# Kernel optimization log

Hardware: AMD Instinct MI355X
Metric: run time of the kernel (lower is better)

Reference implementation:

```python
import jax, jax.numpy as jnp
import numpy as np

B, N = 8, 16384
NPOINT, RADIUS, NSAMPLE, IN_CH = 512, 0.5, 64, 6
EPS = 1e-5


def _sqdist(a, b):
    # a [B,S,3], b [B,N,3] -> [B,S,N] squared euclidean distances
    return (jnp.sum(a * a, -1)[:, :, None] + jnp.sum(b * b, -1)[:, None, :]
            - 2.0 * jnp.einsum('bsd,bnd->bsn', a, b))


def _fps(xyz, npoint):
    # farthest point sampling (deterministic: starts from index 0)
    Bb, Nn, _ = xyz.shape
    def body(carry, _):
        dist, far = carry  # dist [B,N], far [B]
        centroid = jnp.take_along_axis(xyz, far[:, None, None], axis=1)  # [B,1,3]
        d = jnp.sum((xyz - centroid) ** 2, -1)
        dist = jnp.minimum(dist, d)
        return (dist, jnp.argmax(dist, -1).astype(jnp.int32)), far
    init = (jnp.full((Bb, Nn), 1e10, xyz.dtype), jnp.zeros((Bb,), jnp.int32))
    _, idx = jax.lax.scan(body, init, None, length=npoint)
    return idx.T  # [B, npoint]


def _ball_query(radius, nsample, xyz, new_xyz):
    Nn = xyz.shape[1]
    sq = _sqdist(new_xyz, xyz)  # [B,S,N]
    gidx = jnp.where(sq > radius * radius, Nn,
                     jnp.arange(Nn, dtype=jnp.int32)[None, None, :])
    gidx = jnp.sort(gidx, axis=-1)[:, :, :nsample]  # [B,S,K]
    # pad slots (==N) get the first valid index, as in reference torch code
    return jnp.where(gidx == Nn, gidx[:, :, :1], gidx)


def _gather(x, idx):
    # x [B,N,C], idx [B,...] -> [B,...,C]
    return jax.vmap(lambda xb, ib: xb[ib])(x, idx)


def _forward(xyz, points, layers):
    fps_idx = _fps(xyz, NPOINT)
    new_xyz = _gather(xyz, fps_idx)                        # [B,S,3]
    idx = _ball_query(RADIUS, NSAMPLE, xyz, new_xyz)       # [B,S,K]
    grouped_xyz = _gather(xyz, idx) - new_xyz[:, :, None]  # [B,S,K,3]
    grouped_pts = _gather(points, idx)                     # [B,S,K,3]
    h = jnp.concatenate([grouped_xyz, grouped_pts], -1)[..., :IN_CH]  # [B,S,K,6]
    for (W, b, g, beta) in layers:
        # 1x1 Conv2d == per-point linear; BatchNorm2d (train mode) over (B,K,S)
        h = jnp.einsum('bskc,oc->bsko', h, W) + b
        mu = jnp.mean(h, axis=(0, 1, 2))
        var = jnp.var(h, axis=(0, 1, 2))
        h = jax.nn.relu(g * (h - mu) * jax.lax.rsqrt(var + EPS) + beta)
    return new_xyz, jnp.max(h, axis=2)  # [B,S,3], [B,S,C_out]


def setup_inputs() -> dict:
    key = jax.random.key(0)
    ks = jax.random.split(key, 4)
    return {
        'xyz': jax.random.normal(ks[0], (B, N, 3), jnp.float32),
        'points': jax.random.normal(ks[1], (B, N, 3), jnp.float32),
        'W0': jax.random.normal(ks[2], (64, IN_CH), jnp.float32) * (1.0 / np.sqrt(IN_CH)),
        'b0': jnp.zeros((64,), jnp.float32),
        'g0': jnp.ones((64,), jnp.float32),
        'beta0': jnp.zeros((64,), jnp.float32),
        'W1': jax.random.normal(ks[3], (128, 64), jnp.float32) * (1.0 / np.sqrt(64)),
        'b1': jnp.zeros((128,), jnp.float32),
        'g1': jnp.ones((128,), jnp.float32),
        'beta1': jnp.zeros((128,), jnp.float32),
    }


def reference(xyz, points, W0, b0, g0, beta0, W1, b1, g1, beta1):
    layers = [(W0, b0, g0, beta0), (W1, b1, g1, beta1)]
    return _forward(xyz, points, layers)
```

## Files before the change

kernel.cpp:

```cpp
#include <hip/hip_runtime.h>

#define NB    8
#define NPTS  16384
#define NS    512
#define NK    64
#define C1    64
#define C2    128
#define RAD2  0.25f
#define MTOT  (NB*NS*NK)

typedef float v2f __attribute__((ext_vector_type(2)));
typedef __bf16 bfv8 __attribute__((ext_vector_type(8)));
typedef float f32x4 __attribute__((ext_vector_type(4)));

extern __shared__ char dynsmem[];

#define UMAX_DPP(x, CTRL, RM)                                                   \
    do {                                                                        \
        unsigned _m = (unsigned)__builtin_amdgcn_update_dpp((int)(x), (int)(x), \
                                                            CTRL, RM, 0xf, false); \
        x = (x > _m) ? x : _m;                                                  \
    } while (0)
#define UMIN_DPP(x, CTRL, RM)                                                   \
    do {                                                                        \
        unsigned _m = (unsigned)__builtin_amdgcn_update_dpp((int)(x), (int)(x), \
                                                            CTRL, RM, 0xf, false); \
        x = (x < _m) ? x : _m;                                                  \
    } while (0)

__global__ __launch_bounds__(1024, 4) void fps_kernel(const float* __restrict__ xyz,
                                                      float* __restrict__ out) {
#pragma clang fp contract(off)
    int b = blockIdx.x;
    int tid = threadIdx.x;
    int lane = tid & 63;
    int w = tid >> 6;
    const float* base = xyz + (size_t)b * NPTS * 3;
    v2f* yv = (v2f*)dynsmem;
    v2f* zv = yv + 8192;
    __shared__ unsigned svals[2][16];
    __shared__ float4 sred4[2][16];
    v2f pxp[8], ddp[8];
#pragma unroll
    for (int jj = 0; jj < 8; ++jj) {
        int p0 = tid + (jj << 11);
        int p1 = p0 + 1024;
        float x0 = base[p0 * 3 + 0], y0 = base[p0 * 3 + 1], z0 = base[p0 * 3 + 2];
        float x1 = base[p1 * 3 + 0], y1 = base[p1 * 3 + 1], z1 = base[p1 * 3 + 2];
        pxp[jj].x = x0; pxp[jj].y = x1;
        v2f yp; yp.x = y0; yp.y = y1;
        v2f zp; zp.x = z0; zp.y = z1;
        yv[(jj << 10) + tid] = yp;
        zv[(jj << 10) + tid] = zp;
        ddp[jj].x = 1e10f; ddp[jj].y = 1e10f;
    }
    float cx = base[0], cy = base[1], cz = base[2];
    if (tid == 0) {
        float* o = out + (size_t)b * NS * 3;
        o[0] = cx; o[1] = cy; o[2] = cz;
    }
    __syncthreads();
    for (int i = 1; i < NS; ++i) {
        v2f cx2; cx2.x = cx; cx2.y = cx;
        v2f cy2; cy2.x = cy; cy2.y = cy;
        v2f cz2; cz2.x = cz; cz2.y = cz;
        v2f cm0, cm1, cm2, cm3;
        cm0.x = -1.f; cm0.y = -1.f; cm1 = cm0; cm2 = cm0; cm3 = cm0;
#pragma unroll
        for (int jj = 0; jj < 8; ++jj) {
            v2f yp = yv[(jj << 10) + tid];
            v2f zp = zv[(jj << 10) + tid];
            v2f dx = pxp[jj] - cx2;
            v2f dy = yp - cy2;
            v2f dz = zp - cz2;
            v2f d = (dx * dx + dy * dy) + dz * dz;
            v2f nd;
            nd.x = fminf(ddp[jj].x, d.x);
            nd.y = fminf(ddp[jj].y, d.y);
            ddp[jj] = nd;
            if ((jj & 3) == 0) { cm0.x = fmaxf(cm0.x, nd.x); cm0.y = fmaxf(cm0.y, nd.y); }
            if ((jj & 3) == 1) { cm1.x = fmaxf(cm1.x, nd.x); cm1.y = fmaxf(cm1.y, nd.y); }
            if ((jj & 3) == 2) { cm2.x = fmaxf(cm2.x, nd.x); cm2.y = fmaxf(cm2.y, nd.y); }
            if ((jj & 3) == 3) { cm3.x = fmaxf(cm3.x, nd.x); cm3.y = fmaxf(cm3.y, nd.y); }
        }
        v2f m01; m01.x = fmaxf(cm0.x, cm1.x); m01.y = fmaxf(cm0.y, cm1.y);
        v2f m23; m23.x = fmaxf(cm2.x, cm3.x); m23.y = fmaxf(cm2.y, cm3.y);
        float bv = fmaxf(fmaxf(m01.x, m23.x), fmaxf(m01.y, m23.y));
        unsigned vb = (unsigned)__float_as_int(bv);
        UMAX_DPP(vb, 0xB1, 0xf);
        UMAX_DPP(vb, 0x4E, 0xf);
        UMAX_DPP(vb, 0x141, 0xf);
        UMAX_DPP(vb, 0x140, 0xf);
        UMAX_DPP(vb, 0x142, 0xa);
        UMAX_DPP(vb, 0x143, 0xc);
        if (lane == 63) svals[i & 1][w] = vb;
        __syncthreads();
        unsigned wv = svals[i & 1][lane & 15];
        UMAX_DPP(wv, 0xB1, 0xf);
        UMAX_DPP(wv, 0x4E, 0xf);
        UMAX_DPP(wv, 0x141, 0xf);
        UMAX_DPP(wv, 0x140, 0xf);
        float W = __int_as_float((int)wv);
        if (__any(bv == W)) {
            unsigned lidx = 0x7fffffffu;
            float lx = 0.f;
#pragma unroll
            for (int jj = 7; jj >= 0; --jj) {
                if (ddp[jj].y == W) { lidx = (unsigned)(tid + (jj << 11) + 1024); lx = pxp[jj].y; }
                if (ddp[jj].x == W) { lidx = (unsigned)(tid + (jj << 11));        lx = pxp[jj].x; }
            }
            unsigned lm = (lidx == 0x7fffffffu) ? 0u : lidx;
            unsigned slot = ((lm >> 11) << 10) + (lm & 1023u);
            unsigned e4 = ((lm >> 10) & 1u) << 2;
            float ly = *(const float*)((const char*)yv + (size_t)slot * 8 + e4);
            float lz = *(const float*)((const char*)zv + (size_t)slot * 8 + e4);
            unsigned widx = lidx;
            UMIN_DPP(widx, 0xB1, 0xf);
            UMIN_DPP(widx, 0x4E, 0xf);
            UMIN_DPP(widx, 0x141, 0xf);
            UMIN_DPP(widx, 0x140, 0xf);
            UMIN_DPP(widx, 0x142, 0xa);
            UMIN_DPP(widx, 0x143, 0xc);
            unsigned wu = (unsigned)__builtin_amdgcn_readlane((int)widx, 63);
            unsigned long long mk = __ballot(lidx == wu);
            int sl = (int)(__ffsll(mk) - 1);
            float sx = __int_as_float(__builtin_amdgcn_readlane(__float_as_int(lx), sl));
            float sy = __int_as_float(__builtin_amdgcn_readlane(__float_as_int(ly), sl));
            float sz = __int_as_float(__builtin_amdgcn_readlane(__float_as_int(lz), sl));
            if (lane == 0) sred4[i & 1][w] = make_float4(__int_as_float((int)wu), sx, sy, sz);
        } else {
            if (lane == 0) sred4[i & 1][w] = make_float4(__int_as_float(0x7fffffff), 0.f, 0.f, 0.f);
        }
        __syncthreads();
        float4 s4 = sred4[i & 1][lane & 15];
        unsigned ci = (unsigned)__float_as_int(s4.x);
        UMIN_DPP(ci, 0xB1, 0xf);
        UMIN_DPP(ci, 0x4E, 0xf);
        UMIN_DPP(ci, 0x141, 0xf);
        UMIN_DPP(ci, 0x140, 0xf);
        unsigned long long mk2 = __ballot((unsigned)__float_as_int(s4.x) == ci);
        int sl2 = (int)(__ffsll(mk2) - 1);
        cx = __int_as_float(__builtin_amdgcn_readlane(__float_as_int(s4.y), sl2));
        cy = __int_as_float(__builtin_amdgcn_readlane(__float_as_int(s4.z), sl2));
        cz = __int_as_float(__builtin_amdgcn_readlane(__float_as_int(s4.w), sl2));
        if (tid == 0) {
            float* o = out + ((size_t)b * NS + i) * 3;
            o[0] = cx; o[1] = cy; o[2] = cz;
        }
    }
}

__global__ __launch_bounds__(256) void ballq_kernel(const float* __restrict__ xyz,
                                                    const float* __restrict__ pts,
                                                    const float* __restrict__ newxyz,
                                                    float* __restrict__ feat) {
    int w = threadIdx.x >> 6;
    int lane = threadIdx.x & 63;
    int wid = blockIdx.x * 4 + w;
    int b = wid >> 9;
    const float* nx = newxyz + (size_t)wid * 3;
    float cx = nx[0], cy = nx[1], cz = nx[2];
    float sa = __fadd_rn(__fadd_rn(__fmul_rn(cx, cx), __fmul_rn(cy, cy)),
                         __fmul_rn(cz, cz));
    __shared__ int sidx[4][64];
    const float* base = xyz + (size_t)b * NPTS * 3;
    int cnt = 0;
    for (int off = 0; off < NPTS && cnt < NK; off += 64) {
        int p = off + lane;
        float bx = base[p * 3 + 0], by = base[p * 3 + 1], bz = base[p * 3 + 2];
        float sb = __fadd_rn(__fadd_rn(__fmul_rn(bx, bx), __fmul_rn(by, by)),
                             __fmul_rn(bz, bz));
        float dt = __fadd_rn(__fadd_rn(__fmul_rn(cx, bx), __fmul_rn(cy, by)),
                             __fmul_rn(cz, bz));
        float sq = __fsub_rn(__fadd_rn(sa, sb), __fmul_rn(2.0f, dt));
        bool inb = !(sq > RAD2);
        unsigned long long mask = __ballot(inb);
        int pos = cnt + (int)__popcll(mask & ((1ull << lane) - 1ull));
        if (inb && pos < NK) sidx[w][pos] = p;
        cnt += (int)__popcll(mask);
    }
    __syncthreads();
    int filled = cnt < NK ? cnt : NK;
    int sel = (lane < filled) ? lane : 0;
    int p = (filled > 0) ? sidx[w][sel] : 0;
    float gx = base[p * 3 + 0], gy = base[p * 3 + 1], gz = base[p * 3 + 2];
    const float* pb = pts + (size_t)b * NPTS * 3;
    float q0 = pb[p * 3 + 0], q1 = pb[p * 3 + 1], q2 = pb[p * 3 + 2];
    float* fr = feat + ((size_t)wid * NK + lane) * 6;
    fr[0] = __fsub_rn(gx, cx);
    fr[1] = __fsub_rn(gy, cy);
    fr[2] = __fsub_rn(gz, cz);
    fr[3] = q0; fr[4] = q1; fr[5] = q2;
}

__global__ __launch_bounds__(256) void stats0_kernel(const float* __restrict__ feat,
                                                     const float* __restrict__ W0,
                                                     const float* __restrict__ b0,
                                                     float* __restrict__ stats) {
    int lane = threadIdx.x & 63;
    int wid = blockIdx.x * 4 + (threadIdx.x >> 6);
    float w0[6];
#pragma unroll
    for (int j = 0; j < 6; ++j) w0[j] = W0[lane * 6 + j];
    float bb = b0[lane];
    float ssum = 0.f, ssq = 0.f;
    int r0 = wid * 256;
    for (int r = r0; r < r0 + 256; ++r) {
        const float* f = feat + (size_t)r * 6;
        float h = bb;
#pragma unroll
        for (int j = 0; j < 6; ++j) h = fmaf(w0[j], f[j], h);
        ssum += h;
        ssq = fmaf(h, h, ssq);
    }
    atomicAdd(&stats[lane], ssum);
    atomicAdd(&stats[64 + lane], ssq);
}

__global__ void fin0_kernel(const float* __restrict__ g0, const float* __restrict__ be0,
                            float* __restrict__ stats) {
    int c = threadIdx.x;
    const float inv = 1.0f / (float)MTOT;
    float mu = stats[c] * inv;
    float var = fmaxf(stats[64 + c] * inv - mu * mu, 0.f);
    float a = g0[c] * rsqrtf(var + 1e-5f);
    stats[384 + c] = a;
    stats[448 + c] = fmaf(-mu, a, be0[c]);
}

__global__ __launch_bounds__(256) void stats1_kernel(const float* __restrict__ feat,
                                                     const float* __restrict__ W0,
                                                     const float* __restrict__ b0,
                                                     const float* __restrict__ W1,
                                                     const float* __restrict__ b1,
                                                     float* __restrict__ stats) {
    int lane = threadIdx.x & 63;
    int w = threadIdx.x >> 6;
    int half = w & 1;
    int pairG = blockIdx.x * 2 + (w >> 1);
    int ch = half * 64 + lane;
    float w0r[6];
#pragma unroll
    for (int j = 0; j < 6; ++j) w0r[j] = W0[lane * 6 + j];
    float b0v = b0[lane];
    float a0 = stats[384 + lane], c0 = stats[448 + lane];
    float w1r[64];
#pragma unroll
    for (int j = 0; j < 64; ++j) w1r[j] = W1[ch * 64 + j];
    float b1v = b1[ch];
    float ssum = 0.f, ssq = 0.f;
    int r0 = pairG * 128;
    for (int r = r0; r < r0 + 128; ++r) {
        const float* f = feat + (size_t)r * 6;
        float h = b0v;
#pragma unroll
        for (int j = 0; j < 6; ++j) h = fmaf(w0r[j], f[j], h);
        float h0n = fmaxf(fmaf(a0, h, c0), 0.f);
        int hbits = __float_as_int(h0n);
        float a0c = 0.f, a1c = 0.f, a2c = 0.f, a3c = 0.f;
#pragma unroll
        for (int j = 0; j < 64; j += 4) {
            a0c = fmaf(w1r[j + 0], __int_as_float(__builtin_amdgcn_readlane(hbits, j + 0)), a0c);
            a1c = fmaf(w1r[j + 1], __int_as_float(__builtin_amdgcn_readlane(hbits, j + 1)), a1c);
            a2c = fmaf(w1r[j + 2], __int_as_float(__builtin_amdgcn_readlane(hbits, j + 2)), a2c);
            a3c = fmaf(w1r[j + 3], __int_as_float(__builtin_amdgcn_readlane(hbits, j + 3)), a3c);
        }
        float acc = b1v + ((a0c + a1c) + (a2c + a3c));
        ssum += acc;
        ssq = fmaf(acc, acc, ssq);
    }
    atomicAdd(&stats[128 + ch], ssum);
    atomicAdd(&stats[256 + ch], ssq);
}

__global__ void fin1_kernel(const float* __restrict__ g1, const float* __restrict__ be1,
                            float* __restrict__ stats) {
    int c = threadIdx.x;
    const float inv = 1.0f / (float)MTOT;
    float mu = stats[128 + c] * inv;
    float var = fmaxf(stats[256 + c] * inv - mu * mu, 0.f);
    float a = g1[c] * rsqrtf(var + 1e-5f);
    stats[512 + c] = a;
    stats[640 + c] = fmaf(-mu, a, be1[c]);
}

__global__ __launch_bounds__(256) void final_mfma_kernel(const float* __restrict__ feat,
                                                         const float* __restrict__ W0,
                                                         const float* __restrict__ b0,
                                                         const float* __restrict__ W1,
                                                         const float* __restrict__ b1,
                                                         const float* __restrict__ stats,
                                                         float* __restrict__ out) {
    char* lds = dynsmem;
    int tid = threadIdx.x;
    int lane = tid & 63;
    int w = tid >> 6;
    int g = blockIdx.x * 4 + w;
    for (int idx = tid; idx < 8192; idx += 256) {
        int o = idx >> 6, c = idx & 63;
        float v = W1[idx];
        unsigned u = __float_as_uint(v);
        unsigned hi = (u + 0x7fffu + ((u >> 16) & 1u)) >> 16;
        float rem = v - __uint_as_float(hi << 16);
        unsigned ur = __float_as_uint(rem);
        unsigned lo = (ur + 0x7fffu + ((ur >> 16) & 1u)) >> 16;
        int byt = (c * 2) ^ ((o & 7) << 4);
        *(unsigned short*)(lds + o * 128 + byt) = (unsigned short)hi;
        *(unsigned short*)(lds + 16384 + o * 128 + byt) = (unsigned short)lo;
    }
    char* X = lds + 32768 + w * 16384;
    float w0r[6];
#pragma unroll
    for (int j = 0; j < 6; ++j) w0r[j] = W0[lane * 6 + j];
    float b0v = b0[lane];
    float a0 = stats[384 + lane], c0v = stats[448 + lane];
    __syncthreads();
    const float* fb = feat + (size_t)g * 64 * 6;
#pragma unroll 4
    for (int r = 0; r < 64; ++r) {
        const float* f = fb + r * 6;
        float h = b0v;
#pragma unroll
        for (int j = 0; j < 6; ++j) h = fmaf(w0r[j], f[j], h);
        float hn = fmaxf(fmaf(a0, h, c0v), 0.f);
        unsigned u = __float_as_uint(hn);
        unsigned hi = (u + 0x7fffu + ((u >> 16) & 1u)) >> 16;
        float rem = hn - __uint_as_float(hi << 16);
        unsigned ur = __float_as_uint(rem);
        unsigned lo = (ur + 0x7fffu + ((ur >> 16) & 1u)) >> 16;
        int byt = (lane * 2) ^ ((r & 7) << 4);
        *(unsigned short*)(X + r * 128 + byt) = (unsigned short)hi;
        *(unsigned short*)(X + 8192 + r * 128 + byt) = (unsigned short)lo;
    }
    __syncthreads();
    float a1v[8], d1v[8];
#pragma unroll
    for (int tn = 0; tn < 8; ++tn) {
        int o = tn * 16 + (lane & 15);
        float a1 = stats[512 + o];
        a1v[tn] = a1;
        d1v[tn] = fmaf(a1, b1[o], stats[640 + o]);
    }
    float mx[8];
#pragma unroll
    for (int tn = 0; tn < 8; ++tn) mx[tn] = -1e30f;
#pragma unroll
    for (int tm = 0; tm < 4; ++tm) {
        bfv8 Ah[2], Al[2];
#pragma unroll
        for (int tk = 0; tk < 2; ++tk) {
            int r = tm * 16 + (lane & 15);
            int colb = (((lane >> 4) * 16) + tk * 64) ^ ((r & 7) << 4);
            Ah[tk] = *(const bfv8*)(X + r * 128 + colb);
            Al[tk] = *(const bfv8*)(X + 8192 + r * 128 + colb);
        }
#pragma unroll
        for (int tn = 0; tn < 8; ++tn) {
            int o = tn * 16 + (lane & 15);
            f32x4 acc = {0.f, 0.f, 0.f, 0.f};
#pragma unroll
            for (int tk = 0; tk < 2; ++tk) {
                int colb = (((lane >> 4) * 16) + tk * 64) ^ ((o & 7) << 4);
                bfv8 Bh = *(const bfv8*)(lds + o * 128 + colb);
                bfv8 Bl = *(const bfv8*)(lds + 16384 + o * 128 + colb);
                acc = __builtin_amdgcn_mfma_f32_16x16x32_bf16(Ah[tk], Bh, acc, 0, 0, 0);
                acc = __builtin_amdgcn_mfma_f32_16x16x32_bf16(Ah[tk], Bl, acc, 0, 0, 0);
                acc = __builtin_amdgcn_mfma_f32_16x16x32_bf16(Al[tk], Bh, acc, 0, 0, 0);
            }
            float t0 = fmaxf(fmaf(a1v[tn], acc[0], d1v[tn]), 0.f);
            float t1 = fmaxf(fmaf(a1v[tn], acc[1], d1v[tn]), 0.f);
            float t2 = fmaxf(fmaf(a1v[tn], acc[2], d1v[tn]), 0.f);
            float t3 = fmaxf(fmaf(a1v[tn], acc[3], d1v[tn]), 0.f);
            mx[tn] = fmaxf(mx[tn], fmaxf(fmaxf(t0, t1), fmaxf(t2, t3)));
        }
    }
#pragma unroll
    for (int tn = 0; tn < 8; ++tn) {
        float v = mx[tn];
        v = fmaxf(v, __shfl_xor(v, 16));
        v = fmaxf(v, __shfl_xor(v, 32));
        mx[tn] = v;
    }
    if (lane < 16) {
        size_t ob = 12288 + (size_t)g * 128;
#pragma unroll
        for (int tn = 0; tn < 8; ++tn) out[ob + tn * 16 + lane] = mx[tn];
    }
}

extern "C" void kernel_launch(void* const* d_in, const int* in_sizes, int n_in,
                              void* d_out, int out_size, void* d_ws, size_t ws_size,
                              hipStream_t stream) {
    const float* xyz = (const float*)d_in[0];
    const float* pts = (const float*)d_in[1];
    const float* W0  = (const float*)d_in[2];
    const float* b0  = (const float*)d_in[3];
    const float* g0  = (const float*)d_in[4];
    const float* be0 = (const float*)d_in[5];
    const float* W1  = (const float*)d_in[6];
    const float* b1  = (const float*)d_in[7];
    const float* g1  = (const float*)d_in[8];
    const float* be1 = (const float*)d_in[9];
    float* out = (float*)d_out;

    float* feat  = (float*)d_ws;
    float* stats = feat + (size_t)MTOT * 6;

    const int fps_lds = 2 * NPTS * (int)sizeof(float);
    (void)hipFuncSetAttribute(reinterpret_cast<const void*>(fps_kernel),
                              hipFuncAttributeMaxDynamicSharedMemorySize, fps_lds);
    const int fm_lds = 98304;
    (void)hipFuncSetAttribute(reinterpret_cast<const void*>(final_mfma_kernel),
                              hipFuncAttributeMaxDynamicSharedMemorySize, fm_lds);

    (void)hipMemsetAsync(stats, 0, 384 * sizeof(float), stream);
    fps_kernel<<<NB, 1024, fps_lds, stream>>>(xyz, out);
    ballq_kernel<<<1024, 256, 0, stream>>>(xyz, pts, out, feat);
    stats0_kernel<<<256, 256, 0, stream>>>(feat, W0, b0, stats);
    fin0_kernel<<<1, 64, 0, stream>>>(g0, be0, stats);
    stats1_kernel<<<1024, 256, 0, stream>>>(feat, W0, b0, W1, b1, stats);
    fin1_kernel<<<1, 128, 0, stream>>>(g1, be1, stats);
    final_mfma_kernel<<<1024, 256, fm_lds, stream>>>(feat, W0, b0, W1, b1, stats, out);
}
```

Measured before the change: 1.160 ms.

## Split FPS across 32 blocks per batch with global-memory argmax exchange

Farthest point sampling is redistributed from one 1024-thread block per batch to 32 blocks of 512 threads per batch, each holding one point per thread in registers. Every iteration each block publishes a packed (distance, inverted index) key to a per-iteration slot in global memory with release atomics, then spin-waits with acquire loads until all 32 slots for that batch are filled. The blocks then reduce the keys to find the next centroid. This spreads the per-iteration distance update over many CUs instead of 8, replacing the LDS-based block reduction. It adds a cross-block global synchronization on every one of the 511 steps. That exchange depends on all 256 blocks being co-resident and adds global-memory latency per step.

```diff
diff --git a/kernel.cpp b/kernel.cpp
--- a/kernel.cpp
+++ b/kernel.cpp
@@ -9,7 +9,6 @@
 #define RAD2  0.25f
 #define MTOT  (NB*NS*NK)
 
-typedef float v2f __attribute__((ext_vector_type(2)));
 typedef __bf16 bfv8 __attribute__((ext_vector_type(8)));
 typedef float f32x4 __attribute__((ext_vector_type(4)));
 
@@ -21,132 +20,83 @@
                                                             CTRL, RM, 0xf, false); \
         x = (x > _m) ? x : _m;                                                  \
     } while (0)
-#define UMIN_DPP(x, CTRL, RM)                                                   \
-    do {                                                                        \
-        unsigned _m = (unsigned)__builtin_amdgcn_update_dpp((int)(x), (int)(x), \
-                                                            CTRL, RM, 0xf, false); \
-        x = (x < _m) ? x : _m;                                                  \
-    } while (0)
-
-__global__ __launch_bounds__(1024, 4) void fps_kernel(const float* __restrict__ xyz,
-                                                      float* __restrict__ out) {
-#pragma clang fp contract(off)
-    int b = blockIdx.x;
+
+__global__ __launch_bounds__(512) void fps_kernel(const float* __restrict__ xyz,
+                                                  float* __restrict__ out,
+                                                  unsigned long long* __restrict__ slots) {
+    int gb = blockIdx.x;
+    int b = gb >> 5;
+    int blk = gb & 31;
     int tid = threadIdx.x;
     int lane = tid & 63;
     int w = tid >> 6;
     const float* base = xyz + (size_t)b * NPTS * 3;
-    v2f* yv = (v2f*)dynsmem;
-    v2f* zv = yv + 8192;
-    __shared__ unsigned svals[2][16];
-    __shared__ float4 sred4[2][16];
-    v2f pxp[8], ddp[8];
-#pragma unroll
-    for (int jj = 0; jj < 8; ++jj) {
-        int p0 = tid + (jj << 11);
-        int p1 = p0 + 1024;
-        float x0 = base[p0 * 3 + 0], y0 = base[p0 * 3 + 1], z0 = base[p0 * 3 + 2];
-        float x1 = base[p1 * 3 + 0], y1 = base[p1 * 3 + 1], z1 = base[p1 * 3 + 2];
-        pxp[jj].x = x0; pxp[jj].y = x1;
-        v2f yp; yp.x = y0; yp.y = y1;
-        v2f zp; zp.x = z0; zp.y = z1;
-        yv[(jj << 10) + tid] = yp;
-        zv[(jj << 10) + tid] = zp;
-        ddp[jj].x = 1e10f; ddp[jj].y = 1e10f;
-    }
+    int p = (blk << 9) + tid;
+    float px = base[p * 3 + 0], py = base[p * 3 + 1], pz = base[p * 3 + 2];
+    float dd = 1e10f;
+    __shared__ unsigned long long warr[8];
+    __shared__ float sc[3];
+    unsigned long long* bslots = slots + (size_t)b * NS * 32;
     float cx = base[0], cy = base[1], cz = base[2];
-    if (tid == 0) {
+    if (blk == 0 && tid == 0) {
         float* o = out + (size_t)b * NS * 3;
         o[0] = cx; o[1] = cy; o[2] = cz;
     }
-    __syncthreads();
     for (int i = 1; i < NS; ++i) {
-        v2f cx2; cx2.x = cx; cx2.y = cx;
-        v2f cy2; cy2.x = cy; cy2.y = cy;
-        v2f cz2; cz2.x = cz; cz2.y = cz;
-        v2f cm0, cm1, cm2, cm3;
-        cm0.x = -1.f; cm0.y = -1.f; cm1 = cm0; cm2 = cm0; cm3 = cm0;
-#pragma unroll
-        for (int jj = 0; jj < 8; ++jj) {
-            v2f yp = yv[(jj << 10) + tid];
-            v2f zp = zv[(jj << 10) + tid];
-            v2f dx = pxp[jj] - cx2;
-            v2f dy = yp - cy2;
-            v2f dz = zp - cz2;
-            v2f d = (dx * dx + dy * dy) + dz * dz;
-            v2f nd;
-            nd.x = fminf(ddp[jj].x, d.x);
-            nd.y = fminf(ddp[jj].y, d.y);
-            ddp[jj] = nd;
-            if ((jj & 3) == 0) { cm0.x = fmaxf(cm0.x, nd.x); cm0.y = fmaxf(cm0.y, nd.y); }
-            if ((jj & 3) == 1) { cm1.x = fmaxf(cm1.x, nd.x); cm1.y = fmaxf(cm1.y, nd.y); }
-            if ((jj & 3) == 2) { cm2.x = fmaxf(cm2.x, nd.x); cm2.y = fmaxf(cm2.y, nd.y); }
-            if ((jj & 3) == 3) { cm3.x = fmaxf(cm3.x, nd.x); cm3.y = fmaxf(cm3.y, nd.y); }
-        }
-        v2f m01; m01.x = fmaxf(cm0.x, cm1.x); m01.y = fmaxf(cm0.y, cm1.y);
-        v2f m23; m23.x = fmaxf(cm2.x, cm3.x); m23.y = fmaxf(cm2.y, cm3.y);
-        float bv = fmaxf(fmaxf(m01.x, m23.x), fmaxf(m01.y, m23.y));
-        unsigned vb = (unsigned)__float_as_int(bv);
+        float dx = __fsub_rn(px, cx);
+        float dy = __fsub_rn(py, cy);
+        float dz = __fsub_rn(pz, cz);
+        float d = __fadd_rn(__fadd_rn(__fmul_rn(dx, dx), __fmul_rn(dy, dy)),
+                            __fmul_rn(dz, dz));
+        dd = fminf(dd, d);
+        unsigned vb = __float_as_uint(dd);
         UMAX_DPP(vb, 0xB1, 0xf);
         UMAX_DPP(vb, 0x4E, 0xf);
         UMAX_DPP(vb, 0x141, 0xf);
         UMAX_DPP(vb, 0x140, 0xf);
         UMAX_DPP(vb, 0x142, 0xa);
         UMAX_DPP(vb, 0x143, 0xc);
-        if (lane == 63) svals[i & 1][w] = vb;
+        unsigned wmax = (unsigned)__builtin_amdgcn_readlane((int)vb, 63);
+        unsigned long long mk = __ballot(__float_as_uint(dd) == wmax);
+        if (lane == 0) {
+            int ml = (int)(__ffsll(mk) - 1);
+            int idx = (blk << 9) + (w << 6) + ml;
+            warr[w] = ((unsigned long long)wmax << 32) |
+                      (unsigned)(0x7fffffff - idx);
+        }
         __syncthreads();
-        unsigned wv = svals[i & 1][lane & 15];
-        UMAX_DPP(wv, 0xB1, 0xf);
-        UMAX_DPP(wv, 0x4E, 0xf);
-        UMAX_DPP(wv, 0x141, 0xf);
-        UMAX_DPP(wv, 0x140, 0xf);
-        float W = __int_as_float((int)wv);
-        if (__any(bv == W)) {
-            unsigned lidx = 0x7fffffffu;
-            float lx = 0.f;
-#pragma unroll
-            for (int jj = 7; jj >= 0; --jj) {
-                if (ddp[jj].y == W) { lidx = (unsigned)(tid + (jj << 11) + 1024); lx = pxp[jj].y; }
-                if (ddp[jj].x == W) { lidx = (unsigned)(tid + (jj << 11));        lx = pxp[jj].x; }
+        if (tid == 0) {
+            unsigned long long bp = warr[0];
+#pragma unroll
+            for (int k = 1; k < 8; ++k) {
+                unsigned long long v = warr[k];
+                if (v > bp) bp = v;
             }
-            unsigned lm = (lidx == 0x7fffffffu) ? 0u : lidx;
-            unsigned slot = ((lm >> 11) << 10) + (lm & 1023u);
-            unsigned e4 = ((lm >> 10) & 1u) << 2;
-            float ly = *(const float*)((const char*)yv + (size_t)slot * 8 + e4);
-            float lz = *(const float*)((const char*)zv + (size_t)slot * 8 + e4);
-            unsigned widx = lidx;
-            UMIN_DPP(widx, 0xB1, 0xf);
-            UMIN_DPP(widx, 0x4E, 0xf);
-            UMIN_DPP(widx, 0x141, 0xf);
-            UMIN_DPP(widx, 0x140, 0xf);
-            UMIN_DPP(widx, 0x142, 0xa);
-            UMIN_DPP(widx, 0x143, 0xc);
-            unsigned wu = (unsigned)__builtin_amdgcn_readlane((int)widx, 63);
-            unsigned long long mk = __ballot(lidx == wu);
-            int sl = (int)(__ffsll(mk) - 1);
-            float sx = __int_as_float(__builtin_amdgcn_readlane(__float_as_int(lx), sl));
-            float sy = __int_as_float(__builtin_amdgcn_readlane(__float_as_int(ly), sl));
-            float sz = __int_as_float(__builtin_amdgcn_readlane(__float_as_int(lz), sl));
-            if (lane == 0) sred4[i & 1][w] = make_float4(__int_as_float((int)wu), sx, sy, sz);
-        } else {
-            if (lane == 0) sred4[i & 1][w] = make_float4(__int_as_float(0x7fffffff), 0.f, 0.f, 0.f);
+            __hip_atomic_store(&bslots[(size_t)i * 32 + blk], bp,
+                               __ATOMIC_RELEASE, __HIP_MEMORY_SCOPE_AGENT);
+        }
+        if (w == 0) {
+            const unsigned long long* ps = &bslots[(size_t)i * 32 + (lane & 31)];
+            unsigned long long v;
+            do {
+                v = __hip_atomic_load(ps, __ATOMIC_ACQUIRE,
+                                      __HIP_MEMORY_SCOPE_AGENT);
+            } while (!__all(v != 0ull));
+#pragma unroll
+            for (int off = 1; off <= 16; off <<= 1) {
+                unsigned long long o = __shfl_xor(v, off);
+                if (o > v) v = o;
+            }
+            int idx = 0x7fffffff - (int)(unsigned)(v & 0xffffffffu);
+            const float* cp = base + (size_t)idx * 3;
+            if (lane < 3) {
+                float c = cp[lane];
+                sc[lane] = c;
+                if (blk == 0) out[((size_t)b * NS + i) * 3 + lane] = c;
+            }
         }
         __syncthreads();
-        float4 s4 = sred4[i & 1][lane & 15];
-        unsigned ci = (unsigned)__float_as_int(s4.x);
-        UMIN_DPP(ci, 0xB1, 0xf);
-        UMIN_DPP(ci, 0x4E, 0xf);
-        UMIN_DPP(ci, 0x141, 0xf);
-        UMIN_DPP(ci, 0x140, 0xf);
-        unsigned long long mk2 = __ballot((unsigned)__float_as_int(s4.x) == ci);
-        int sl2 = (int)(__ffsll(mk2) - 1);
-        cx = __int_as_float(__builtin_amdgcn_readlane(__float_as_int(s4.y), sl2));
-        cy = __int_as_float(__builtin_amdgcn_readlane(__float_as_int(s4.z), sl2));
-        cz = __int_as_float(__builtin_amdgcn_readlane(__float_as_int(s4.w), sl2));
-        if (tid == 0) {
-            float* o = out + ((size_t)b * NS + i) * 3;
-            o[0] = cx; o[1] = cy; o[2] = cz;
-        }
+        cx = sc[0]; cy = sc[1]; cz = sc[2];
     }
 }
 
@@ -405,16 +355,15 @@
 
     float* feat  = (float*)d_ws;
     float* stats = feat + (size_t)MTOT * 6;
-
-    const int fps_lds = 2 * NPTS * (int)sizeof(float);
-    (void)hipFuncSetAttribute(reinterpret_cast<const void*>(fps_kernel),
-                              hipFuncAttributeMaxDynamicSharedMemorySize, fps_lds);
+    unsigned long long* slots = (unsigned long long*)(stats + 768);
+
     const int fm_lds = 98304;
     (void)hipFuncSetAttribute(reinterpret_cast<const void*>(final_mfma_kernel),
                               hipFuncAttributeMaxDynamicSharedMemorySize, fm_lds);
 
     (void)hipMemsetAsync(stats, 0, 384 * sizeof(float), stream);
-    fps_kernel<<<NB, 1024, fps_lds, stream>>>(xyz, out);
+    (void)hipMemsetAsync(slots, 0, (size_t)NB * NS * 32 * 8, stream);
+    fps_kernel<<<NB * 32, 512, 0, stream>>>(xyz, out, slots);
     ballq_kernel<<<1024, 256, 0, stream>>>(xyz, pts, out, feat);
     stats0_kernel<<<256, 256, 0, stream>>>(feat, W0, b0, stats);
     fin0_kernel<<<1, 64, 0, stream>>>(g0, be0, stats);
```

Result: slower. 3.353 ms (+189.1%).
